# Kernel tuning notes

Hardware: AMD Instinct MI355X
Metric: run time of the kernel (lower is better)

The kernel has to match this reference:

```python
import jax, jax.numpy as jnp
import numpy as np

ALPHA = 1.0

def setup_inputs() -> dict:
    key = jax.random.key(0)
    X = jax.random.normal(key, (8192, 64), dtype=jnp.float32)
    return {"X": X}

def reference(X) -> jnp.ndarray:
    # Pairwise squared L2 distances via GEMM trick: ||x_i||^2 + ||x_j||^2 - 2 x_i.x_j
    sq = jnp.sum(X * X, axis=1)                      # [N]
    d2 = sq[:, None] + sq[None, :] - 2.0 * (X @ X.T)  # [N, N]
    d2 = jnp.maximum(d2, 0.0)
    # sigma^2 = alpha * mean(d2), detached (no grad through bandwidth)
    sigma_sq = ALPHA * jax.lax.stop_gradient(jnp.mean(d2))
    return jnp.exp(-d2 / (2.0 * sigma_sq))
```

## Files before the change

### kernel.cpp

```cpp
#include <hip/hip_runtime.h>
#include <hip/hip_bf16.h>

#define N 8192
#define D 64

typedef __attribute__((ext_vector_type(8))) short bf16x8;
typedef __attribute__((ext_vector_type(4))) float f32x4;

__device__ inline unsigned short f2b(float f) {
    __hip_bfloat16 h = __float2bfloat16(f);
    return __builtin_bit_cast(unsigned short, h);
}

__device__ inline float exp2fast(float x) {
#if __has_builtin(__builtin_amdgcn_exp2f)
    return __builtin_amdgcn_exp2f(x);
#else
    return exp2f(x);
#endif
}

__global__ __launch_bounds__(256) void gk_prep(const float4* __restrict__ X4,
                                               ushort4* __restrict__ Xb4,
                                               float* __restrict__ sq,
                                               float4* __restrict__ Vp4) {
    __shared__ float4 sm[256];
    const int tid = threadIdx.x;
    const int g = blockIdx.x * 256 + tid;
    float4 v = X4[g];
    ushort4 b;
    b.x = f2b(v.x); b.y = f2b(v.y); b.z = f2b(v.z); b.w = f2b(v.w);
    Xb4[g] = b;
    float ss = v.x * v.x + v.y * v.y + v.z * v.z + v.w * v.w;
    ss += __shfl_xor(ss, 8, 16);
    ss += __shfl_xor(ss, 4, 16);
    ss += __shfl_xor(ss, 2, 16);
    ss += __shfl_xor(ss, 1, 16);
    if ((tid & 15) == 0) sq[g >> 4] = ss;
    sm[tid] = v;
    __syncthreads();
#pragma unroll
    for (int off = 128; off >= 16; off >>= 1) {
        if (tid < off) {
            float4 o = sm[tid + off];
            float4 m = sm[tid];
            m.x += o.x; m.y += o.y; m.z += o.z; m.w += o.w;
            sm[tid] = m;
        }
        __syncthreads();
    }
    if (tid < 16) Vp4[blockIdx.x * 16 + tid] = sm[tid];
}

__global__ __launch_bounds__(256) void gk_finalize(const float* __restrict__ sq,
                                                   const float* __restrict__ Vp,
                                                   float* __restrict__ scal,
                                                   float4* __restrict__ u4) {
    __shared__ float red[256];
    const int tid = threadIdx.x;
    float s = 0.f;
    for (int r = tid; r < N; r += 256) s += sq[r];
    red[tid] = s;
    __syncthreads();
    for (int off = 128; off > 0; off >>= 1) {
        if (tid < off) red[tid] += red[tid + off];
        __syncthreads();
    }
    const float S = red[0];
    __syncthreads();
    const int c = tid & 63, p = tid >> 6;
    float v = 0.f;
    for (int r = p; r < 512; r += 4) v += Vp[r * 64 + c];
    red[tid] = v;
    __syncthreads();
    if (tid < 128) red[tid] += red[tid + 128];
    __syncthreads();
    if (tid < 64) red[tid] += red[tid + 64];
    __syncthreads();
    float vv = (tid < 64) ? red[tid] * red[tid] : 0.f;
    __syncthreads();
    red[tid] = vv;
    __syncthreads();
    for (int off = 128; off > 0; off >>= 1) {
        if (tid < off) red[tid] += red[tid + off];
        __syncthreads();
    }
    if (tid == 0) {
        const float Vsq = red[0];
        const float fN = (float)N;
        const float mean = 2.f * S / fN - 2.f * Vsq / (fN * fN);
        const float sc = 1.f / (2.f * mean);
        const float L2E = 1.4426950408889634f;
        scal[0] = sc;
        scal[1] = 2.f * sc * L2E;
        red[0] = sc * L2E;
    }
    __syncthreads();
    const float uc = red[0];
    const float4* sqv = reinterpret_cast<const float4*>(sq);
    for (int r = tid; r < N / 4; r += 256) {
        float4 q = sqv[r];
        float4 o;
        o.x = q.x * uc; o.y = q.y * uc; o.z = q.z * uc; o.w = q.w * uc;
        u4[r] = o;
    }
}

__global__ __launch_bounds__(256) void gk_main(const unsigned short* __restrict__ Xb,
                                               const float* __restrict__ u,
                                               const float* __restrict__ scal,
                                               float* __restrict__ out) {
    __shared__ float lds[4][16][128];
    const int lane = threadIdx.x & 63;
    const int wave = threadIdx.x >> 6;
    const int i0 = blockIdx.y * 64 + wave * 16;
    const int j0 = blockIdx.x * 128;
    const int m = lane & 15;
    const int q = lane >> 4;
    const float k2 = scal[1];

    const bf16x8* Brow = reinterpret_cast<const bf16x8*>(Xb + (i0 + m) * D + 8 * q);
    const bf16x8 b0 = Brow[0];
    const bf16x8 b1 = Brow[4];

    f32x4 acc[8];
#pragma unroll
    for (int t = 0; t < 8; ++t) acc[t] = (f32x4){0.f, 0.f, 0.f, 0.f};

#pragma unroll
    for (int t = 0; t < 8; ++t) {
        const bf16x8* Arow =
            reinterpret_cast<const bf16x8*>(Xb + (j0 + t * 16 + m) * D + 8 * q);
        acc[t] = __builtin_amdgcn_mfma_f32_16x16x32_bf16(Arow[0], b0, acc[t], 0, 0, 0);
        acc[t] = __builtin_amdgcn_mfma_f32_16x16x32_bf16(Arow[4], b1, acc[t], 0, 0, 0);
    }

    const float ui = u[i0 + m];
    const f32x4* u4 = reinterpret_cast<const f32x4*>(u + j0 + 4 * q);
    float* ldsrow = &lds[wave][m][0];

#pragma unroll
    for (int t = 0; t < 8; ++t) {
        const f32x4 uj = u4[t * 4];
        f32x4 e;
#pragma unroll
        for (int r = 0; r < 4; ++r) {
            const float s = ui + uj[r];
            const float pz = fmaf(k2, acc[t][r], -s);
            e[r] = exp2fast(fminf(pz, 0.f));
        }
        const int cs = (16 * t + 4 * q + 4 * m) & 127;
        *reinterpret_cast<f32x4*>(ldsrow + cs) = e;
    }

    const int half = lane >> 5;
    const int c = (lane & 31) * 4;
#pragma unroll
    for (int p = 0; p < 8; ++p) {
        const int r = 2 * p + half;
        const int cr = (c + 4 * r) & 127;
        const f32x4 v = *reinterpret_cast<const f32x4*>(&lds[wave][r][cr]);
        *reinterpret_cast<f32x4*>(out + (size_t)(i0 + r) * N + j0 + c) = v;
    }
}

extern "C" void kernel_launch(void* const* d_in, const int* in_sizes, int n_in,
                              void* d_out, int out_size, void* d_ws, size_t ws_size,
                              hipStream_t stream) {
    const float* X = (const float*)d_in[0];
    float* out = (float*)d_out;

    char* ws = (char*)d_ws;
    unsigned short* Xb = (unsigned short*)ws;
    float* sq = (float*)(ws + (1 << 20));
    float* Vp = (float*)(ws + (1 << 20) + (32 << 10));
    float* u  = (float*)(ws + (1 << 20) + (160 << 10));
    float* scal = (float*)(ws + (1 << 20) + (192 << 10));

    gk_prep<<<512, 256, 0, stream>>>((const float4*)X, (ushort4*)Xb, sq, (float4*)Vp);
    gk_finalize<<<1, 256, 0, stream>>>(sq, Vp, scal, (float4*)u);

    dim3 grid(N / 128, N / 64);
    gk_main<<<grid, 256, 0, stream>>>(Xb, u, scal, out);
}
```

Before: 334.4 us.

## Swap MFMA operand roles to store output directly without LDS transpose

Swaps the A/B operand roles of the MFMA so each lane's accumulator values land on output columns indexed by lane, then writes them straight to global memory and drops the LDS staging buffer and its transpose pass. The grid is also transposed so consecutive blocks walk along rows instead of columns. This removes the LDS round trip and its synchronisation cost, but the stores become scalar 4-byte writes of 64 bytes per row segment rather than 16-byte vector stores, which may lower write efficiency on this store-bound kernel.

Result: no change. 332.7 us (-0.5%).

```diff
diff --git a/kernel.cpp b/kernel.cpp
--- a/kernel.cpp
+++ b/kernel.cpp
@@ -110,18 +110,17 @@
                                                const float* __restrict__ u,
                                                const float* __restrict__ scal,
                                                float* __restrict__ out) {
-    __shared__ float lds[4][16][128];
     const int lane = threadIdx.x & 63;
     const int wave = threadIdx.x >> 6;
-    const int i0 = blockIdx.y * 64 + wave * 16;
-    const int j0 = blockIdx.x * 128;
+    const int i0 = blockIdx.x * 64 + wave * 16;
+    const int j0 = blockIdx.y * 128;
     const int m = lane & 15;
     const int q = lane >> 4;
     const float k2 = scal[1];
 
-    const bf16x8* Brow = reinterpret_cast<const bf16x8*>(Xb + (i0 + m) * D + 8 * q);
-    const bf16x8 b0 = Brow[0];
-    const bf16x8 b1 = Brow[4];
+    const bf16x8* Arow = reinterpret_cast<const bf16x8*>(Xb + (i0 + m) * D + 8 * q);
+    const bf16x8 a0 = Arow[0];
+    const bf16x8 a1 = Arow[4];
 
     f32x4 acc[8];
 #pragma unroll
@@ -129,38 +128,27 @@
 
 #pragma unroll
     for (int t = 0; t < 8; ++t) {
-        const bf16x8* Arow =
+        const bf16x8* Brow =
             reinterpret_cast<const bf16x8*>(Xb + (j0 + t * 16 + m) * D + 8 * q);
-        acc[t] = __builtin_amdgcn_mfma_f32_16x16x32_bf16(Arow[0], b0, acc[t], 0, 0, 0);
-        acc[t] = __builtin_amdgcn_mfma_f32_16x16x32_bf16(Arow[4], b1, acc[t], 0, 0, 0);
+        const bf16x8 b0 = Brow[0];
+        const bf16x8 b1 = Brow[4];
+        acc[t] = __builtin_amdgcn_mfma_f32_16x16x32_bf16(a0, b0, acc[t], 0, 0, 0);
+        acc[t] = __builtin_amdgcn_mfma_f32_16x16x32_bf16(a1, b1, acc[t], 0, 0, 0);
     }
 
-    const float ui = u[i0 + m];
-    const f32x4* u4 = reinterpret_cast<const f32x4*>(u + j0 + 4 * q);
-    float* ldsrow = &lds[wave][m][0];
+    float ui[4];
+#pragma unroll
+    for (int r = 0; r < 4; ++r) ui[r] = u[i0 + 4 * q + r];
 
 #pragma unroll
     for (int t = 0; t < 8; ++t) {
-        const f32x4 uj = u4[t * 4];
-        f32x4 e;
+        const int col = j0 + t * 16 + m;
+        const float uj = u[col];
 #pragma unroll
         for (int r = 0; r < 4; ++r) {
-            const float s = ui + uj[r];
-            const float pz = fmaf(k2, acc[t][r], -s);
-            e[r] = exp2fast(fminf(pz, 0.f));
+            const float pz = fmaf(k2, acc[t][r], -(ui[r] + uj));
+            out[(size_t)(i0 + 4 * q + r) * N + col] = exp2fast(fminf(pz, 0.f));
         }
-        const int cs = (16 * t + 4 * q + 4 * m) & 127;
-        *reinterpret_cast<f32x4*>(ldsrow + cs) = e;
-    }
-
-    const int half = lane >> 5;
-    const int c = (lane & 31) * 4;
-#pragma unroll
-    for (int p = 0; p < 8; ++p) {
-        const int r = 2 * p + half;
-        const int cr = (c + 4 * r) & 127;
-        const f32x4 v = *reinterpret_cast<const f32x4*>(&lds[wave][r][cr]);
-        *reinterpret_cast<f32x4*>(out + (size_t)(i0 + r) * N + j0 + c) = v;
     }
 }
 
@@ -180,6 +168,6 @@
     gk_prep<<<512, 256, 0, stream>>>((const float4*)X, (ushort4*)Xb, sq, (float4*)Vp);
     gk_finalize<<<1, 256, 0, stream>>>(sq, Vp, scal, (float4*)u);
 
-    dim3 grid(N / 128, N / 64);
+    dim3 grid(N / 64, N / 128);
     gk_main<<<grid, 256, 0, stream>>>(Xb, u, scal, out);
 }
```
